# Performance work log

Measured on AMD Instinct MI355X. Metric: run time of the kernel, lower is better.

## Reference

```python
import jax, jax.numpy as jnp
import numpy as np

B = 262144
IN = 256
HID = 128
OUT = 15
C = 15  # num_cameras


def setup_inputs() -> dict:
    key = jax.random.key(0)
    k_x, k_c, k_w1, k_b1, k_w2, k_b2 = jax.random.split(key, 6)
    x = jax.random.normal(k_x, (B, IN), dtype=jnp.float32)
    cam = jax.random.randint(k_c, (B,), 0, C)
    # per-camera 2-layer MLP params (Linear->ReLU->Dropout(eval)->Linear)
    W1 = jax.random.normal(k_w1, (C, IN, HID), dtype=jnp.float32) / np.sqrt(IN)
    b1 = jax.random.normal(k_b1, (C, HID), dtype=jnp.float32) * 0.01
    W2 = jax.random.normal(k_w2, (C, HID, OUT), dtype=jnp.float32) / np.sqrt(HID)
    b2 = jax.random.normal(k_b2, (C, OUT), dtype=jnp.float32) * 0.01
    return {"input": x, "cam": cam, "W1": W1, "b1": b1, "W2": W2, "b2": b2}


def reference(input, cam, W1, b1, W2, b2):
    # Per-sample camera-id dispatch to one of C small MLPs, vectorized:
    # run each camera's MLP on the full batch (C is small/fixed) and select
    # each sample's output by its camera id. Dropout is identity (eval mode).
    out = jnp.zeros((input.shape[0], OUT), dtype=input.dtype)
    for c in range(C):
        h = jax.nn.relu(input @ W1[c] + b1[c])      # [B, HID]
        logits = h @ W2[c] + b2[c]                  # [B, OUT]
        out = jnp.where((cam == c)[:, None], logits, out)
    return out
```

## Files before the change

kernel.cpp:

```cpp
#include <hip/hip_runtime.h>
#include <hip/hip_bf16.h>

#define BB    262144
#define INF   256
#define HIDF  128
#define OUTF  15
#define NCAM  15
#define TM    128
#define MAXTILES (BB/TM + NCAM)

typedef __attribute__((ext_vector_type(8))) short          bf16x8;
typedef __attribute__((ext_vector_type(4))) float          floatx4;
typedef __attribute__((ext_vector_type(4))) int            intx4;
typedef __attribute__((ext_vector_type(4))) unsigned int   uintx4;
typedef __attribute__((ext_vector_type(8))) unsigned short ushortx8;

__device__ __forceinline__ unsigned short f2bf1(float a){
  unsigned int u = __builtin_bit_cast(unsigned int, a);
  u += 0x7fffu + ((u >> 16) & 1u);
  return (unsigned short)(u >> 16);
}
__device__ __forceinline__ unsigned int f2bf2(float a, float b){
  return (unsigned int)f2bf1(a) | ((unsigned int)f2bf1(b) << 16);
}

__global__ void k_prep(const float* __restrict__ W1, const float* __restrict__ W2,
                       unsigned short* __restrict__ W1p, unsigned short* __restrict__ W2p,
                       int* __restrict__ counts, int* __restrict__ scatterOfs){
  int bid = blockIdx.x, tid = threadIdx.x;
  if (bid < 240){
    int t = bid * 256 + tid;
    int l  = t & 63;
    int kf = (t >> 6) & 7;
    int nf = (t >> 9) & 7;
    int c  = t >> 12;
    int col = nf*16 + (l & 15);
    int k0  = kf*32 + (l >> 4)*8;
    ushortx8 v;
    #pragma unroll
    for (int j = 0; j < 8; ++j)
      v[j] = f2bf1(W1[((size_t)c*INF + k0 + j)*HIDF + col]);
    *reinterpret_cast<ushortx8*>(W1p + (size_t)t*8) = v;
  } else if (bid < 255){
    int c  = bid - 240;
    int l  = tid & 63;
    int kf = tid >> 6;
    int col = l & 15;
    int k0  = kf*32 + (l >> 4)*8;
    ushortx8 v;
    #pragma unroll
    for (int j = 0; j < 8; ++j){
      float f = (col < OUTF) ? W2[((size_t)c*HIDF + k0 + j)*OUTF + col] : 0.0f;
      v[j] = f2bf1(f);
    }
    *reinterpret_cast<ushortx8*>(W2p + ((size_t)(c*4 + kf)*64 + l)*8) = v;
  } else {
    if (tid < 16) counts[tid] = 0;
    else if (tid < 32) scatterOfs[tid - 16] = 0;
  }
}

__global__ void k_hist(const int* __restrict__ cam, int* __restrict__ counts){
  __shared__ int lc[NCAM];
  int t = threadIdx.x;
  if (t < NCAM) lc[t] = 0;
  __syncthreads();
  intx4 v = *reinterpret_cast<const intx4*>(cam + (size_t)(blockIdx.x*256 + t)*4);
  atomicAdd(&lc[v[0]], 1); atomicAdd(&lc[v[1]], 1);
  atomicAdd(&lc[v[2]], 1); atomicAdd(&lc[v[3]], 1);
  __syncthreads();
  if (t < NCAM && lc[t]) atomicAdd(&counts[t], lc[t]);
}

__global__ void k_scatter(const int* __restrict__ cam, const int* __restrict__ counts,
                          int* __restrict__ scatterOfs, int* __restrict__ idx){
  __shared__ int lc[NCAM];
  __shared__ int loff[NCAM];
  __shared__ int base[NCAM];
  int t = threadIdx.x;
  if (t < NCAM) lc[t] = 0;
  __syncthreads();
  int start = blockIdx.x * 4096;
  int camr[16], lpos[16];
  #pragma unroll
  for (int j = 0; j < 16; ++j){
    int i = start + j*256 + t;
    camr[j] = cam[i];
    lpos[j] = atomicAdd(&lc[camr[j]], 1);
  }
  __syncthreads();
  if (t == 0){
    int s = 0;
    #pragma unroll
    for (int c = 0; c < NCAM; ++c){ loff[c] = s; s += counts[c]; }
  }
  __syncthreads();
  if (t < NCAM) base[t] = loff[t] + atomicAdd(&scatterOfs[t], lc[t]);
  __syncthreads();
  #pragma unroll
  for (int j = 0; j < 16; ++j)
    idx[base[camr[j]] + lpos[j]] = start + j*256 + t;
}

__global__ __launch_bounds__(256, 2) void k_mlp(
    const float* __restrict__ x, const int* __restrict__ idx,
    const int* __restrict__ counts,
    const unsigned short* __restrict__ W1p, const unsigned short* __restrict__ W2p,
    const float* __restrict__ b1, const float* __restrict__ b2,
    float* __restrict__ out)
{
  __shared__ int sidx[TM];
  __shared__ unsigned short hbuf[TM][HIDF];

  int bid = blockIdx.x;
  int c = -1, segStart = 0, rowStart = 0, rows = 0;
  {
    int cum = 0, rcum = 0;
    #pragma unroll 1
    for (int cc = 0; cc < NCAM; ++cc){
      int n  = counts[cc];
      int nt = (n + TM - 1) / TM;
      if (c < 0 && bid < cum + nt){
        c = cc;
        rowStart = (bid - cum) * TM;
        segStart = rcum;
        rows = n - rowStart; if (rows > TM) rows = TM;
      }
      cum += nt; rcum += n;
    }
  }
  if (c < 0) return;

  int t = threadIdx.x;
  if (t < TM){
    int r = (t < rows) ? t : (rows - 1);
    sidx[t] = idx[segStart + rowStart + r];
  }
  __syncthreads();

  int wave = t >> 6, lane = t & 63;
  int wr  = wave * 32;
  int l15 = lane & 15, lk = lane >> 4;

  const float* ap0 = x + (size_t)sidx[wr + l15]      * INF + lk*8;
  const float* ap1 = x + (size_t)sidx[wr + 16 + l15] * INF + lk*8;
  const unsigned short* bbase = W1p + (size_t)c*32768 + lane*8;

  floatx4 acc[2][8];
  #pragma unroll
  for (int i = 0; i < 2; ++i)
    #pragma unroll
    for (int j = 0; j < 8; ++j) acc[i][j] = (floatx4)0.0f;

  floatx4 a[3][4];
  bf16x8  bfr[2][8];

  #pragma unroll
  for (int s = 0; s < 3; ++s){
    a[s][0] = *reinterpret_cast<const floatx4*>(ap0 + s*32);
    a[s][1] = *reinterpret_cast<const floatx4*>(ap0 + s*32 + 4);
    a[s][2] = *reinterpret_cast<const floatx4*>(ap1 + s*32);
    a[s][3] = *reinterpret_cast<const floatx4*>(ap1 + s*32 + 4);
  }
  #pragma unroll
  for (int nf = 0; nf < 8; ++nf)
    bfr[0][nf] = *reinterpret_cast<const bf16x8*>(bbase + nf*4096);

  #pragma unroll
  for (int kf = 0; kf < 8; ++kf){
    const int cur  = kf % 3;
    const int bcur = kf & 1;
    if (kf < 7){
      #pragma unroll
      for (int nf = 0; nf < 8; ++nf)
        bfr[bcur^1][nf] = *reinterpret_cast<const bf16x8*>(bbase + nf*4096 + (kf+1)*512);
    }
    uintx4 u0, u1;
    u0[0] = f2bf2(a[cur][0][0], a[cur][0][1]); u0[1] = f2bf2(a[cur][0][2], a[cur][0][3]);
    u0[2] = f2bf2(a[cur][1][0], a[cur][1][1]); u0[3] = f2bf2(a[cur][1][2], a[cur][1][3]);
    u1[0] = f2bf2(a[cur][2][0], a[cur][2][1]); u1[1] = f2bf2(a[cur][2][2], a[cur][2][3]);
    u1[2] = f2bf2(a[cur][3][0], a[cur][3][1]); u1[3] = f2bf2(a[cur][3][2], a[cur][3][3]);
    bf16x8 af0 = __builtin_bit_cast(bf16x8, u0);
    bf16x8 af1 = __builtin_bit_cast(bf16x8, u1);
    if (kf < 5){
      a[cur][0] = *reinterpret_cast<const floatx4*>(ap0 + (kf+3)*32);
      a[cur][1] = *reinterpret_cast<const floatx4*>(ap0 + (kf+3)*32 + 4);
      a[cur][2] = *reinterpret_cast<const floatx4*>(ap1 + (kf+3)*32);
      a[cur][3] = *reinterpret_cast<const floatx4*>(ap1 + (kf+3)*32 + 4);
    }
    #pragma unroll
    for (int nf = 0; nf < 8; ++nf)
      acc[0][nf] = __builtin_amdgcn_mfma_f32_16x16x32_bf16(af0, bfr[bcur][nf], acc[0][nf], 0, 0, 0);
    #pragma unroll
    for (int nf = 0; nf < 8; ++nf)
      acc[1][nf] = __builtin_amdgcn_mfma_f32_16x16x32_bf16(af1, bfr[bcur][nf], acc[1][nf], 0, 0, 0);
  }

  #pragma unroll
  for (int nf = 0; nf < 8; ++nf){
    int col = nf*16 + l15;
    float bias = b1[c*HIDF + col];
    #pragma unroll
    for (int mf = 0; mf < 2; ++mf){
      #pragma unroll
      for (int j = 0; j < 4; ++j){
        int row = wr + mf*16 + lk*4 + j;
        float h = fmaxf(acc[mf][nf][j] + bias, 0.0f);
        int cb = (col*2) ^ ((row & 7) << 4);
        *reinterpret_cast<unsigned short*>(
            reinterpret_cast<char*>(&hbuf[row][0]) + cb) = f2bf1(h);
      }
    }
  }
  __syncthreads();

  floatx4 acc2[2];
  acc2[0] = (floatx4)0.0f; acc2[1] = (floatx4)0.0f;
  const unsigned short* wb = W2p + (size_t)c*2048 + lane*8;
  #pragma unroll
  for (int kf = 0; kf < 4; ++kf){
    bf16x8 wv = *reinterpret_cast<const bf16x8*>(wb + kf*512);
    #pragma unroll
    for (int mf = 0; mf < 2; ++mf){
      int row = wr + mf*16 + l15;
      int cb = (kf*64 + lk*16) ^ ((row & 7) << 4);
      bf16x8 av = *reinterpret_cast<const bf16x8*>(
          reinterpret_cast<char*>(&hbuf[row][0]) + cb);
      acc2[mf] = __builtin_amdgcn_mfma_f32_16x16x32_bf16(av, wv, acc2[mf], 0, 0, 0);
    }
  }

  int col = l15;
  if (col < OUTF){
    float bias2 = b2[c*OUTF + col];
    #pragma unroll
    for (int mf = 0; mf < 2; ++mf){
      #pragma unroll
      for (int j = 0; j < 4; ++j){
        int r = wr + mf*16 + lk*4 + j;
        if (r < rows)
          out[(size_t)sidx[r]*OUTF + col] = acc2[mf][j] + bias2;
      }
    }
  }
}

extern "C" void kernel_launch(void* const* d_in, const int* in_sizes, int n_in,
                              void* d_out, int out_size, void* d_ws, size_t ws_size,
                              hipStream_t stream) {
  const float* x  = (const float*)d_in[0];
  const int*   cam= (const int*)d_in[1];
  const float* W1 = (const float*)d_in[2];
  const float* b1 = (const float*)d_in[3];
  const float* W2 = (const float*)d_in[4];
  const float* b2 = (const float*)d_in[5];
  float* out = (float*)d_out;

  char* ws = (char*)d_ws;
  int* counts     = (int*)(ws);
  int* scatterOfs = (int*)(ws + 64);
  int* idx        = (int*)(ws + 256);
  unsigned short* W1p = (unsigned short*)(ws + 256 + (size_t)BB*4);
  unsigned short* W2p = W1p + (size_t)NCAM*8*8*64*8;

  hipLaunchKernelGGL(k_prep,    dim3(256),     dim3(256), 0, stream, W1, W2, W1p, W2p, counts, scatterOfs);
  hipLaunchKernelGGL(k_hist,    dim3(256),     dim3(256), 0, stream, cam, counts);
  hipLaunchKernelGGL(k_scatter, dim3(BB/4096), dim3(256), 0, stream, cam, counts, scatterOfs, idx);
  hipLaunchKernelGGL(k_mlp,     dim3(MAXTILES),dim3(256), 0, stream,
                     x, idx, counts, W1p, W2p, b1, b2, out);
}
```

Baseline: 97.87 us.

## Stage W1 tile in LDS via async global_load_lds and fuse prep/hist kernels

Measured after the change: 103.1 us. 1.05x slower.

```diff
diff --git a/kernel.cpp b/kernel.cpp
--- a/kernel.cpp
+++ b/kernel.cpp
@@ -24,9 +24,10 @@
   return (unsigned int)f2bf1(a) | ((unsigned int)f2bf1(b) << 16);
 }
 
-__global__ void k_prep(const float* __restrict__ W1, const float* __restrict__ W2,
-                       unsigned short* __restrict__ W1p, unsigned short* __restrict__ W2p,
-                       int* __restrict__ counts, int* __restrict__ scatterOfs){
+__global__ void k_prephist(const float* __restrict__ W1, const float* __restrict__ W2,
+                           const int* __restrict__ cam,
+                           unsigned short* __restrict__ W1p, unsigned short* __restrict__ W2p,
+                           int* __restrict__ counts){
   int bid = blockIdx.x, tid = threadIdx.x;
   if (bid < 240){
     int t = bid * 256 + tid;
@@ -54,22 +55,16 @@
       v[j] = f2bf1(f);
     }
     *reinterpret_cast<ushortx8*>(W2p + ((size_t)(c*4 + kf)*64 + l)*8) = v;
-  } else {
-    if (tid < 16) counts[tid] = 0;
-    else if (tid < 32) scatterOfs[tid - 16] = 0;
-  }
-}
-
-__global__ void k_hist(const int* __restrict__ cam, int* __restrict__ counts){
-  __shared__ int lc[NCAM];
-  int t = threadIdx.x;
-  if (t < NCAM) lc[t] = 0;
-  __syncthreads();
-  intx4 v = *reinterpret_cast<const intx4*>(cam + (size_t)(blockIdx.x*256 + t)*4);
-  atomicAdd(&lc[v[0]], 1); atomicAdd(&lc[v[1]], 1);
-  atomicAdd(&lc[v[2]], 1); atomicAdd(&lc[v[3]], 1);
-  __syncthreads();
-  if (t < NCAM && lc[t]) atomicAdd(&counts[t], lc[t]);
+  } else if (bid >= 256){
+    __shared__ int lc[NCAM];
+    if (tid < NCAM) lc[tid] = 0;
+    __syncthreads();
+    intx4 v = *reinterpret_cast<const intx4*>(cam + (size_t)((bid-256)*256 + tid)*4);
+    atomicAdd(&lc[v[0]], 1); atomicAdd(&lc[v[1]], 1);
+    atomicAdd(&lc[v[2]], 1); atomicAdd(&lc[v[3]], 1);
+    __syncthreads();
+    if (tid < NCAM && lc[tid]) atomicAdd(&counts[tid], lc[tid]);
+  }
 }
 
 __global__ void k_scatter(const int* __restrict__ cam, const int* __restrict__ counts,
@@ -109,8 +104,8 @@
     const float* __restrict__ b1, const float* __restrict__ b2,
     float* __restrict__ out)
 {
-  __shared__ int sidx[TM];
-  __shared__ unsigned short hbuf[TM][HIDF];
+  __shared__ __align__(16) char smem[65536 + 512];
+  int* sidx = reinterpret_cast<int*>(smem + 65536);
 
   int bid = blockIdx.x;
   int c = -1, segStart = 0, rowStart = 0, rows = 0;
@@ -132,19 +127,30 @@
   if (c < 0) return;
 
   int t = threadIdx.x;
+  int wave = t >> 6, lane = t & 63;
+
+  {
+    const char* gsrc = reinterpret_cast<const char*>(W1p + (size_t)c*32768);
+    #pragma unroll
+    for (int i = 0; i < 16; ++i){
+      int ci = i*4 + wave;
+      __builtin_amdgcn_global_load_lds(
+        (const __attribute__((address_space(1))) unsigned int*)(gsrc + ci*1024 + lane*16),
+        (__attribute__((address_space(3))) unsigned int*)(smem + ci*1024),
+        16, 0, 0);
+    }
+  }
   if (t < TM){
     int r = (t < rows) ? t : (rows - 1);
     sidx[t] = idx[segStart + rowStart + r];
   }
   __syncthreads();
 
-  int wave = t >> 6, lane = t & 63;
   int wr  = wave * 32;
   int l15 = lane & 15, lk = lane >> 4;
 
   const float* ap0 = x + (size_t)sidx[wr + l15]      * INF + lk*8;
   const float* ap1 = x + (size_t)sidx[wr + 16 + l15] * INF + lk*8;
-  const unsigned short* bbase = W1p + (size_t)c*32768 + lane*8;
 
   floatx4 acc[2][8];
   #pragma unroll
@@ -152,29 +158,22 @@
     #pragma unroll
     for (int j = 0; j < 8; ++j) acc[i][j] = (floatx4)0.0f;
 
-  floatx4 a[3][4];
-  bf16x8  bfr[2][8];
-
-  #pragma unroll
-  for (int s = 0; s < 3; ++s){
+  floatx4 a[4][4];
+  #pragma unroll
+  for (int s = 0; s < 4; ++s){
     a[s][0] = *reinterpret_cast<const floatx4*>(ap0 + s*32);
     a[s][1] = *reinterpret_cast<const floatx4*>(ap0 + s*32 + 4);
     a[s][2] = *reinterpret_cast<const floatx4*>(ap1 + s*32);
     a[s][3] = *reinterpret_cast<const floatx4*>(ap1 + s*32 + 4);
   }
-  #pragma unroll
-  for (int nf = 0; nf < 8; ++nf)
-    bfr[0][nf] = *reinterpret_cast<const bf16x8*>(bbase + nf*4096);
 
   #pragma unroll
   for (int kf = 0; kf < 8; ++kf){
-    const int cur  = kf % 3;
-    const int bcur = kf & 1;
-    if (kf < 7){
-      #pragma unroll
-      for (int nf = 0; nf < 8; ++nf)
-        bfr[bcur^1][nf] = *reinterpret_cast<const bf16x8*>(bbase + nf*4096 + (kf+1)*512);
-    }
+    const int cur = kf & 3;
+    bf16x8 bf[8];
+    #pragma unroll
+    for (int nf = 0; nf < 8; ++nf)
+      bf[nf] = *reinterpret_cast<const bf16x8*>(smem + (nf*8 + kf)*1024 + lane*16);
     uintx4 u0, u1;
     u0[0] = f2bf2(a[cur][0][0], a[cur][0][1]); u0[1] = f2bf2(a[cur][0][2], a[cur][0][3]);
     u0[2] = f2bf2(a[cur][1][0], a[cur][1][1]); u0[3] = f2bf2(a[cur][1][2], a[cur][1][3]);
@@ -182,19 +181,21 @@
     u1[2] = f2bf2(a[cur][3][0], a[cur][3][1]); u1[3] = f2bf2(a[cur][3][2], a[cur][3][3]);
     bf16x8 af0 = __builtin_bit_cast(bf16x8, u0);
     bf16x8 af1 = __builtin_bit_cast(bf16x8, u1);
-    if (kf < 5){
-      a[cur][0] = *reinterpret_cast<const floatx4*>(ap0 + (kf+3)*32);
-      a[cur][1] = *reinterpret_cast<const floatx4*>(ap0 + (kf+3)*32 + 4);
-      a[cur][2] = *reinterpret_cast<const floatx4*>(ap1 + (kf+3)*32);
-      a[cur][3] = *reinterpret_cast<const floatx4*>(ap1 + (kf+3)*32 + 4);
+    if (kf < 4){
+      a[cur][0] = *reinterpret_cast<const floatx4*>(ap0 + (kf+4)*32);
+      a[cur][1] = *reinterpret_cast<const floatx4*>(ap0 + (kf+4)*32 + 4);
+      a[cur][2] = *reinterpret_cast<const floatx4*>(ap1 + (kf+4)*32);
+      a[cur][3] = *reinterpret_cast<const floatx4*>(ap1 + (kf+4)*32 + 4);
     }
     #pragma unroll
     for (int nf = 0; nf < 8; ++nf)
-      acc[0][nf] = __builtin_amdgcn_mfma_f32_16x16x32_bf16(af0, bfr[bcur][nf], acc[0][nf], 0, 0, 0);
+      acc[0][nf] = __builtin_amdgcn_mfma_f32_16x16x32_bf16(af0, bf[nf], acc[0][nf], 0, 0, 0);
     #pragma unroll
     for (int nf = 0; nf < 8; ++nf)
-      acc[1][nf] = __builtin_amdgcn_mfma_f32_16x16x32_bf16(af1, bfr[bcur][nf], acc[1][nf], 0, 0, 0);
-  }
+      acc[1][nf] = __builtin_amdgcn_mfma_f32_16x16x32_bf16(af1, bf[nf], acc[1][nf], 0, 0, 0);
+  }
+
+  __syncthreads();
 
   #pragma unroll
   for (int nf = 0; nf < 8; ++nf){
@@ -206,9 +207,8 @@
       for (int j = 0; j < 4; ++j){
         int row = wr + mf*16 + lk*4 + j;
         float h = fmaxf(acc[mf][nf][j] + bias, 0.0f);
-        int cb = (col*2) ^ ((row & 7) << 4);
-        *reinterpret_cast<unsigned short*>(
-            reinterpret_cast<char*>(&hbuf[row][0]) + cb) = f2bf1(h);
+        int off = row*256 + ((col*2) ^ ((row & 7) << 4));
+        *reinterpret_cast<unsigned short*>(smem + off) = f2bf1(h);
       }
     }
   }
@@ -223,9 +223,8 @@
     #pragma unroll
     for (int mf = 0; mf < 2; ++mf){
       int row = wr + mf*16 + l15;
-      int cb = (kf*64 + lk*16) ^ ((row & 7) << 4);
-      bf16x8 av = *reinterpret_cast<const bf16x8*>(
-          reinterpret_cast<char*>(&hbuf[row][0]) + cb);
+      int off = row*256 + ((kf*64 + lk*16) ^ ((row & 7) << 4));
+      bf16x8 av = *reinterpret_cast<const bf16x8*>(smem + off);
       acc2[mf] = __builtin_amdgcn_mfma_f32_16x16x32_bf16(av, wv, acc2[mf], 0, 0, 0);
     }
   }
@@ -263,9 +262,9 @@
   unsigned short* W1p = (unsigned short*)(ws + 256 + (size_t)BB*4);
   unsigned short* W2p = W1p + (size_t)NCAM*8*8*64*8;
 
-  hipLaunchKernelGGL(k_prep,    dim3(256),     dim3(256), 0, stream, W1, W2, W1p, W2p, counts, scatterOfs);
-  hipLaunchKernelGGL(k_hist,    dim3(256),     dim3(256), 0, stream, cam, counts);
-  hipLaunchKernelGGL(k_scatter, dim3(BB/4096), dim3(256), 0, stream, cam, counts, scatterOfs, idx);
-  hipLaunchKernelGGL(k_mlp,     dim3(MAXTILES),dim3(256), 0, stream,
+  (void)hipMemsetAsync(counts, 0, 128, stream);
+  hipLaunchKernelGGL(k_prephist, dim3(512),     dim3(256), 0, stream, W1, W2, cam, W1p, W2p, counts);
+  hipLaunchKernelGGL(k_scatter,  dim3(BB/4096), dim3(256), 0, stream, cam, counts, scatterOfs, idx);
+  hipLaunchKernelGGL(k_mlp,      dim3(MAXTILES),dim3(256), 0, stream,
                      x, idx, counts, W1p, W2p, b1, b2, out);
 }
```
